# Optimization experiments

Measured on AMD Instinct MI355X. Metric: run time of the kernel, lower is better.

The kernel has to match this reference:

```python
import jax, jax.numpy as jnp
import numpy as np

N_NODES = 100000
N_EDGES = 1600000
IN_FEATS = 128
OUT_FEATS = 64
NEG_SLOPE = 0.2


def setup_inputs() -> dict:
    key = jax.random.key(0)
    k1, k2, k3, k4 = jax.random.split(key, 4)
    feat = jax.random.normal(k1, (N_NODES, IN_FEATS), dtype=jnp.float32)
    # xavier_normal-ish scale for the linear weight (torch Linear stores [out, in])
    W = jax.random.normal(k2, (OUT_FEATS, IN_FEATS), dtype=jnp.float32) * (1.0 / np.sqrt(IN_FEATS))
    src = jax.random.randint(k3, (N_EDGES,), 0, N_NODES, dtype=jnp.int32)
    dst = jax.random.randint(k4, (N_EDGES,), 0, N_NODES, dtype=jnp.int32)
    return {"feat": feat, "W": W, "src": src, "dst": dst}


def reference(feat, W, src, dst):
    n_nodes = feat.shape[0]
    # h = Linear(feat) (no bias)
    h = feat @ W.T                                            # [N, out]
    # update_all(copy_src, sum): h_agg[v] = sum_{(u->v)} h[u]
    h_agg = jax.ops.segment_sum(h[src], dst, num_segments=n_nodes)  # [N, out]
    # NOTE: ndata['h'] was overwritten, so edges see the AGGREGATED features
    e = jnp.sum(h_agg[src] * jnp.tanh(h_agg[dst]), axis=1)   # [E]
    e = jnp.where(e > 0, e, NEG_SLOPE * e)                    # leaky_relu
    # edge_softmax: softmax over incoming edges of each destination node
    m = jax.ops.segment_max(e, dst, num_segments=n_nodes)     # [N]
    ex = jnp.exp(e - m[dst])                                  # [E], stable
    s = jax.ops.segment_sum(ex, dst, num_segments=n_nodes)    # [N]
    e_soft = ex / s[dst]                                      # [E]
    return h_agg, e_soft
```

## Files before the change

### kernel.cpp

```cpp
#include <hip/hip_runtime.h>
#include <math.h>

#define IN_FEATS 128
#define OUT_FEATS 64
#define NEG_SLOPE 0.2f
#define MAXD 256
#define BSH 8
#define BNODES (1 << BSH)
#define CHUNK 8192
#define EID_BITS 21

typedef _Float16 half2_t __attribute__((ext_vector_type(2)));
typedef short bf16x8 __attribute__((ext_vector_type(8)));
typedef float f32x4 __attribute__((ext_vector_type(4)));

__device__ __forceinline__ float bf_lo(unsigned u) { return __uint_as_float(u << 16); }
__device__ __forceinline__ float bf_hi(unsigned u) { return __uint_as_float(u & 0xffff0000u); }
__device__ __forceinline__ unsigned short f2bf(float f) {
  unsigned x = __float_as_uint(f);
  x += 0x7fff + ((x >> 16) & 1);
  return (unsigned short)(x >> 16);
}
template <typename T>
__device__ __forceinline__ unsigned h2u(T h) {
  union { T h; unsigned u; } c; c.h = h; return c.u;
}

__global__ __launch_bounds__(256)
void gemm_h_kernel(const float* __restrict__ feat,
                   const float* __restrict__ W,
                   unsigned short* __restrict__ h16, int n_nodes) {
  const int wid    = (blockIdx.x * blockDim.x + threadIdx.x) >> 6;
  const int lane   = threadIdx.x & 63;
  const int nwaves = (gridDim.x * blockDim.x) >> 6;
  const int r16 = lane & 15;
  const int kb  = lane >> 4;

  bf16x8 wf[4][4];
#pragma unroll
  for (int ot = 0; ot < 4; ++ot) {
#pragma unroll
    for (int kc = 0; kc < 4; ++kc) {
      const float* wp = W + (size_t)(ot * 16 + r16) * IN_FEATS + kc * 32 + kb * 8;
      float4 w0 = *reinterpret_cast<const float4*>(wp);
      float4 w1 = *reinterpret_cast<const float4*>(wp + 4);
      bf16x8 f;
      f[0] = (short)f2bf(w0.x); f[1] = (short)f2bf(w0.y);
      f[2] = (short)f2bf(w0.z); f[3] = (short)f2bf(w0.w);
      f[4] = (short)f2bf(w1.x); f[5] = (short)f2bf(w1.y);
      f[6] = (short)f2bf(w1.z); f[7] = (short)f2bf(w1.w);
      wf[ot][kc] = f;
    }
  }

  const int ntiles = (n_nodes + 15) >> 4;
  for (int t = wid; t < ntiles; t += nwaves) {
    const int n0 = t * 16;
    int row = n0 + r16;
    if (row >= n_nodes) row = n_nodes - 1;
    const float* fp = feat + (size_t)row * IN_FEATS + kb * 8;

    bf16x8 af[4];
#pragma unroll
    for (int kc = 0; kc < 4; ++kc) {
      float4 a0 = *reinterpret_cast<const float4*>(fp + kc * 32);
      float4 a1 = *reinterpret_cast<const float4*>(fp + kc * 32 + 4);
      bf16x8 f;
      f[0] = (short)f2bf(a0.x); f[1] = (short)f2bf(a0.y);
      f[2] = (short)f2bf(a0.z); f[3] = (short)f2bf(a0.w);
      f[4] = (short)f2bf(a1.x); f[5] = (short)f2bf(a1.y);
      f[6] = (short)f2bf(a1.z); f[7] = (short)f2bf(a1.w);
      af[kc] = f;
    }

    f32x4 acc[4];
#pragma unroll
    for (int ot = 0; ot < 4; ++ot) acc[ot] = (f32x4){0.f, 0.f, 0.f, 0.f};
#pragma unroll
    for (int ot = 0; ot < 4; ++ot) {
#pragma unroll
      for (int kc = 0; kc < 4; ++kc) {
        acc[ot] = __builtin_amdgcn_mfma_f32_16x16x32_bf16(af[kc], wf[ot][kc],
                                                          acc[ot], 0, 0, 0);
      }
    }

#pragma unroll
    for (int ot = 0; ot < 4; ++ot) {
#pragma unroll
      for (int reg = 0; reg < 4; ++reg) {
        int node = n0 + (lane >> 4) * 4 + reg;
        if (node < n_nodes)
          h16[(size_t)node * OUT_FEATS + ot * 16 + r16] = f2bf(acc[ot][reg]);
      }
    }
  }
}

__global__ __launch_bounds__(256)
void bhist_kernel(const int* __restrict__ dst, int* __restrict__ bcount,
                  int n_edges, int nbuck) {
  __shared__ int hist[512];
  const int t = threadIdx.x;
  for (int i = t; i < nbuck; i += 256) hist[i] = 0;
  __syncthreads();
  const int n4 = n_edges >> 2;
  const int4* dst4 = reinterpret_cast<const int4*>(dst);
  const int base = blockIdx.x * (CHUNK / 4);
#pragma unroll
  for (int i = 0; i < 8; ++i) {
    int idx = base + t + i * 256;
    if (idx < n4) {
      int4 d = dst4[idx];
      atomicAdd(&hist[d.x >> BSH], 1);
      atomicAdd(&hist[d.y >> BSH], 1);
      atomicAdd(&hist[d.z >> BSH], 1);
      atomicAdd(&hist[d.w >> BSH], 1);
    }
  }
  if (blockIdx.x == 0) {
    for (int e = (n4 << 2) + t; e < n_edges; e += 256)
      atomicAdd(&hist[dst[e] >> BSH], 1);
  }
  __syncthreads();
  for (int i = t; i < nbuck; i += 256)
    if (hist[i]) atomicAdd(&bcount[i], hist[i]);
}

__global__ void bscan_kernel(const int* __restrict__ bcount, int* __restrict__ bbase,
                             int* __restrict__ bcursor, int nbuck, int n_edges) {
  __shared__ int tmp[512];
  const int t = threadIdx.x;
  int v = (t < nbuck) ? bcount[t] : 0;
  tmp[t] = v;
  __syncthreads();
  for (int off = 1; off < 512; off <<= 1) {
    int x = (t >= off) ? tmp[t - off] : 0;
    __syncthreads();
    tmp[t] += x;
    __syncthreads();
  }
  if (t < nbuck) { int excl = tmp[t] - v; bbase[t] = excl; bcursor[t] = excl; }
  if (t == 0) bbase[nbuck] = n_edges;
}

__global__ __launch_bounds__(256)
void bscatter_kernel(const int* __restrict__ src, const int* __restrict__ dst,
                     int* __restrict__ bcursor, int2* __restrict__ tmpe,
                     int n_edges, int nbuck) {
  __shared__ int hist[512];
  __shared__ int basech[512];
  __shared__ int offs[512];
  const int t = threadIdx.x;
  const int n4 = n_edges >> 2;
  const int4* src4 = reinterpret_cast<const int4*>(src);
  const int4* dst4 = reinterpret_cast<const int4*>(dst);
  const int base = blockIdx.x * (CHUNK / 4);
  for (int i = t; i < nbuck; i += 256) { hist[i] = 0; offs[i] = 0; }
  __syncthreads();

  int4 sv[8], dv[8];
#pragma unroll
  for (int i = 0; i < 8; ++i) {
    int idx = base + t + i * 256;
    if (idx < n4) {
      sv[i] = src4[idx];
      dv[i] = dst4[idx];
      atomicAdd(&hist[dv[i].x >> BSH], 1);
      atomicAdd(&hist[dv[i].y >> BSH], 1);
      atomicAdd(&hist[dv[i].z >> BSH], 1);
      atomicAdd(&hist[dv[i].w >> BSH], 1);
    } else {
      dv[i].x = -1;
    }
  }
  if (blockIdx.x == 0) {
    for (int e = (n4 << 2) + t; e < n_edges; e += 256)
      atomicAdd(&hist[dst[e] >> BSH], 1);
  }
  __syncthreads();
  for (int i = t; i < nbuck; i += 256)
    if (hist[i]) basech[i] = atomicAdd(&bcursor[i], hist[i]);
  __syncthreads();

#pragma unroll
  for (int i = 0; i < 8; ++i) {
    if (dv[i].x >= 0) {
      int e0 = (base + t + i * 256) << 2;
      int ss[4] = {sv[i].x, sv[i].y, sv[i].z, sv[i].w};
      int dd[4] = {dv[i].x, dv[i].y, dv[i].z, dv[i].w};
#pragma unroll
      for (int j = 0; j < 4; ++j) {
        int b = dd[j] >> BSH;
        int off = atomicAdd(&offs[b], 1);
        int2 v;
        v.x = ss[j];
        v.y = ((dd[j] & (BNODES - 1)) << EID_BITS) | (e0 + j);
        tmpe[basech[b] + off] = v;
      }
    }
  }
  if (blockIdx.x == 0) {
    for (int e = (n4 << 2) + t; e < n_edges; e += 256) {
      int d = dst[e];
      int b = d >> BSH;
      int off = atomicAdd(&offs[b], 1);
      int2 v;
      v.x = src[e];
      v.y = ((d & (BNODES - 1)) << EID_BITS) | e;
      tmpe[basech[b] + off] = v;
    }
  }
}

__global__ __launch_bounds__(256)
void binB_kernel(const int2* __restrict__ tmpe, const int* __restrict__ bbase,
                 int2* __restrict__ edata, int* __restrict__ row_ptr,
                 int n_nodes, int n_edges) {
  __shared__ int cnt[BNODES];
  __shared__ int cur[BNODES];
  const int b = blockIdx.x;
  const int t = threadIdx.x;
  const int beg = bbase[b], end = bbase[b + 1];

  cnt[t] = 0;
  __syncthreads();
  for (int i = beg + t; i < end; i += 256)
    atomicAdd(&cnt[(tmpe[i].y >> EID_BITS) & (BNODES - 1)], 1);
  __syncthreads();

  int v = cnt[t];
  cur[t] = v;
  __syncthreads();
  for (int off = 1; off < BNODES; off <<= 1) {
    int x = (t >= off) ? cur[t - off] : 0;
    __syncthreads();
    cur[t] += x;
    __syncthreads();
  }
  int excl = cur[t] - v;
  int node = b * BNODES + t;
  if (node < n_nodes) row_ptr[node] = beg + excl;
  if (b == 0 && t == 0) row_ptr[n_nodes] = n_edges;
  __syncthreads();
  cur[t] = beg + excl;
  __syncthreads();

  for (int i = beg + t; i < end; i += 256) {
    int2 p = tmpe[i];
    int l = (p.y >> EID_BITS) & (BNODES - 1);
    int pos = atomicAdd(&cur[l], 1);
    int2 o;
    o.x = p.x;
    o.y = p.y & ((1 << EID_BITS) - 1);
    edata[pos] = o;
  }
}

__global__ void agg_kernel(const unsigned* __restrict__ h16u,
                           const int* __restrict__ row_ptr,
                           const int2* __restrict__ edata, float* __restrict__ h_agg,
                           unsigned* __restrict__ a16u, unsigned* __restrict__ t16u,
                           int n_nodes) {
  int tid  = blockIdx.x * blockDim.x + threadIdx.x;
  int node = tid >> 3;
  int fo   = tid & 7;
  if (node >= n_nodes) return;
  int beg = row_ptr[node], end = row_ptr[node + 1];
  float acc[8] = {0.f, 0.f, 0.f, 0.f, 0.f, 0.f, 0.f, 0.f};
  if (beg < end) {
    uint4 v = *reinterpret_cast<const uint4*>(
        h16u + (unsigned)edata[beg].x * 32u + fo * 4);
    for (int i = beg + 1; i < end; ++i) {
      uint4 vn = *reinterpret_cast<const uint4*>(
          h16u + (unsigned)edata[i].x * 32u + fo * 4);
      acc[0] += bf_lo(v.x); acc[1] += bf_hi(v.x);
      acc[2] += bf_lo(v.y); acc[3] += bf_hi(v.y);
      acc[4] += bf_lo(v.z); acc[5] += bf_hi(v.z);
      acc[6] += bf_lo(v.w); acc[7] += bf_hi(v.w);
      v = vn;
    }
    acc[0] += bf_lo(v.x); acc[1] += bf_hi(v.x);
    acc[2] += bf_lo(v.y); acc[3] += bf_hi(v.y);
    acc[4] += bf_lo(v.z); acc[5] += bf_hi(v.z);
    acc[6] += bf_lo(v.w); acc[7] += bf_hi(v.w);
  }
  float4 a, b;
  a.x = acc[0]; a.y = acc[1]; a.z = acc[2]; a.w = acc[3];
  b.x = acc[4]; b.y = acc[5]; b.z = acc[6]; b.w = acc[7];
  float* out = h_agg + (size_t)node * OUT_FEATS + fo * 8;
  *reinterpret_cast<float4*>(out) = a;
  *reinterpret_cast<float4*>(out + 4) = b;

  uint4 pa;
  pa.x = h2u(__builtin_amdgcn_cvt_pkrtz(acc[0], acc[1]));
  pa.y = h2u(__builtin_amdgcn_cvt_pkrtz(acc[2], acc[3]));
  pa.z = h2u(__builtin_amdgcn_cvt_pkrtz(acc[4], acc[5]));
  pa.w = h2u(__builtin_amdgcn_cvt_pkrtz(acc[6], acc[7]));
  *reinterpret_cast<uint4*>(a16u + (unsigned)node * 32u + fo * 4) = pa;

  uint4 pt;
  pt.x = h2u(__builtin_amdgcn_cvt_pkrtz(tanhf(acc[0]), tanhf(acc[1])));
  pt.y = h2u(__builtin_amdgcn_cvt_pkrtz(tanhf(acc[2]), tanhf(acc[3])));
  pt.z = h2u(__builtin_amdgcn_cvt_pkrtz(tanhf(acc[4]), tanhf(acc[5])));
  pt.w = h2u(__builtin_amdgcn_cvt_pkrtz(tanhf(acc[6]), tanhf(acc[7])));
  *reinterpret_cast<uint4*>(t16u + (unsigned)node * 32u + fo * 4) = pt;
}

__global__ __launch_bounds__(256)
void softmax_kernel(const unsigned* __restrict__ a16u, const unsigned* __restrict__ t16u,
                    const int* __restrict__ row_ptr, const int2* __restrict__ edata,
                    float* __restrict__ e_soft, int n_nodes) {
  __shared__ float ebuf[4][MAXD];
  int wid  = (blockIdx.x * blockDim.x + threadIdx.x) >> 6;
  int lane = threadIdx.x & 63;
  int lw   = threadIdx.x >> 6;
  int eo = lane >> 2;
  int fo = lane & 3;
  if (wid >= n_nodes) return;
  int beg = row_ptr[wid], end = row_ptr[wid + 1];
  int deg = end - beg;
  if (deg == 0) return;

  union U { uint4 u; half2_t h[4]; };
  U tc0, tc1;
  tc0.u = *reinterpret_cast<const uint4*>(t16u + (unsigned)wid * 32u + fo * 8);
  tc1.u = *reinterpret_cast<const uint4*>(t16u + (unsigned)wid * 32u + fo * 8 + 4);

  if (deg <= 32) {
    int eA = eo, eB = 16 + eo;
    int idxA = beg + (eA < deg ? eA : deg - 1);
    int idxB = beg + (eB < deg ? eB : deg - 1);
    int2 edA = edata[idxA];
    int2 edB = edata[idxB];
    U a0A, a1A, a0B, a1B;
    a0A.u = *reinterpret_cast<const uint4*>(a16u + (unsigned)edA.x * 32u + fo * 8);
    a1A.u = *reinterpret_cast<const uint4*>(a16u + (unsigned)edA.x * 32u + fo * 8 + 4);
    a0B.u = *reinterpret_cast<const uint4*>(a16u + (unsigned)edB.x * 32u + fo * 8);
    a1B.u = *reinterpret_cast<const uint4*>(a16u + (unsigned)edB.x * 32u + fo * 8 + 4);

    float dA = 0.f, dB = 0.f;
#pragma unroll
    for (int j = 0; j < 4; ++j) {
      dA = __builtin_amdgcn_fdot2(a0A.h[j], tc0.h[j], dA, false);
      dB = __builtin_amdgcn_fdot2(a0B.h[j], tc0.h[j], dB, false);
    }
#pragma unroll
    for (int j = 0; j < 4; ++j) {
      dA = __builtin_amdgcn_fdot2(a1A.h[j], tc1.h[j], dA, false);
      dB = __builtin_amdgcn_fdot2(a1B.h[j], tc1.h[j], dB, false);
    }
#pragma unroll
    for (int off = 1; off < 4; off <<= 1) {
      dA += __shfl_xor(dA, off, 64);
      dB += __shfl_xor(dB, off, 64);
    }
    dA = dA > 0.f ? dA : NEG_SLOPE * dA;
    dB = dB > 0.f ? dB : NEG_SLOPE * dB;
    float mA = (eA < deg) ? dA : -INFINITY;
    float mB = (eB < deg) ? dB : -INFINITY;
    float mx = fmaxf(mA, mB);
#pragma unroll
    for (int off = 4; off < 64; off <<= 1) mx = fmaxf(mx, __shfl_xor(mx, off, 64));
    float xA = (eA < deg) ? expf(dA - mx) : 0.f;
    float xB = (eB < deg) ? expf(dB - mx) : 0.f;
    float sum = xA + xB;
#pragma unroll
    for (int off = 4; off < 64; off <<= 1) sum += __shfl_xor(sum, off, 64);
    float inv = 1.f / sum;
    if (fo == 0) {
      if (eA < deg) e_soft[edA.y] = xA * inv;
      if (eB < deg) e_soft[edB.y] = xB * inv;
    }
  } else if (deg <= MAXD) {
    for (int i0 = 0; i0 < deg; i0 += 16) {
      int e = i0 + eo;
      int idx = beg + (e < deg ? e : deg - 1);
      int2 ed = edata[idx];
      U a0, a1;
      a0.u = *reinterpret_cast<const uint4*>(a16u + (unsigned)ed.x * 32u + fo * 8);
      a1.u = *reinterpret_cast<const uint4*>(a16u + (unsigned)ed.x * 32u + fo * 8 + 4);
      float d = 0.f;
#pragma unroll
      for (int j = 0; j < 4; ++j) d = __builtin_amdgcn_fdot2(a0.h[j], tc0.h[j], d, false);
#pragma unroll
      for (int j = 0; j < 4; ++j) d = __builtin_amdgcn_fdot2(a1.h[j], tc1.h[j], d, false);
#pragma unroll
      for (int off = 1; off < 4; off <<= 1) d += __shfl_xor(d, off, 64);
      if (fo == 0 && e < deg) {
        d = d > 0.f ? d : NEG_SLOPE * d;
        ebuf[lw][e] = d;
      }
    }
    if (deg <= 64) {
      float sc = (lane < deg) ? ebuf[lw][lane] : -INFINITY;
      float mx = sc;
#pragma unroll
      for (int off = 32; off > 0; off >>= 1) mx = fmaxf(mx, __shfl_xor(mx, off, 64));
      float ex = (lane < deg) ? expf(sc - mx) : 0.f;
      float sum = ex;
#pragma unroll
      for (int off = 32; off > 0; off >>= 1) sum += __shfl_xor(sum, off, 64);
      float inv = 1.f / sum;
      if (lane < deg) e_soft[edata[beg + lane].y] = ex * inv;
    } else {
      float mx = -INFINITY;
      for (int i = lane; i < deg; i += 64) mx = fmaxf(mx, ebuf[lw][i]);
#pragma unroll
      for (int off = 32; off > 0; off >>= 1) mx = fmaxf(mx, __shfl_xor(mx, off, 64));
      float sum = 0.f;
      for (int i = lane; i < deg; i += 64) {
        float ex = expf(ebuf[lw][i] - mx);
        ebuf[lw][i] = ex;
        sum += ex;
      }
#pragma unroll
      for (int off = 32; off > 0; off >>= 1) sum += __shfl_xor(sum, off, 64);
      float inv = 1.f / sum;
      for (int i = lane; i < deg; i += 64) e_soft[edata[beg + i].y] = ebuf[lw][i] * inv;
    }
  } else {
    float mx = -INFINITY;
    for (int i0 = 0; i0 < deg; i0 += 16) {
      int e = i0 + eo;
      int idx = beg + (e < deg ? e : deg - 1);
      int2 ed = edata[idx];
      U a0, a1;
      a0.u = *reinterpret_cast<const uint4*>(a16u + (unsigned)ed.x * 32u + fo * 8);
      a1.u = *reinterpret_cast<const uint4*>(a16u + (unsigned)ed.x * 32u + fo * 8 + 4);
      float d = 0.f;
#pragma unroll
      for (int j = 0; j < 4; ++j) d = __builtin_amdgcn_fdot2(a0.h[j], tc0.h[j], d, false);
#pragma unroll
      for (int j = 0; j < 4; ++j) d = __builtin_amdgcn_fdot2(a1.h[j], tc1.h[j], d, false);
#pragma unroll
      for (int off = 1; off < 4; off <<= 1) d += __shfl_xor(d, off, 64);
      d = d > 0.f ? d : NEG_SLOPE * d;
      if (e >= deg) d = -INFINITY;
#pragma unroll
      for (int off = 4; off < 64; off <<= 1) d = fmaxf(d, __shfl_xor(d, off, 64));
      mx = fmaxf(mx, d);
    }
    float sum = 0.f;
    for (int i0 = 0; i0 < deg; i0 += 16) {
      int e = i0 + eo;
      int idx = beg + (e < deg ? e : deg - 1);
      int2 ed = edata[idx];
      U a0, a1;
      a0.u = *reinterpret_cast<const uint4*>(a16u + (unsigned)ed.x * 32u + fo * 8);
      a1.u = *reinterpret_cast<const uint4*>(a16u + (unsigned)ed.x * 32u + fo * 8 + 4);
      float d = 0.f;
#pragma unroll
      for (int j = 0; j < 4; ++j) d = __builtin_amdgcn_fdot2(a0.h[j], tc0.h[j], d, false);
#pragma unroll
      for (int j = 0; j < 4; ++j) d = __builtin_amdgcn_fdot2(a1.h[j], tc1.h[j], d, false);
#pragma unroll
      for (int off = 1; off < 4; off <<= 1) d += __shfl_xor(d, off, 64);
      d = d > 0.f ? d : NEG_SLOPE * d;
      float ex = (e < deg) ? expf(d - mx) : 0.f;
#pragma unroll
      for (int off = 4; off < 64; off <<= 1) ex += __shfl_xor(ex, off, 64);
      sum += ex;
    }
    float inv = 1.f / sum;
    for (int i0 = 0; i0 < deg; i0 += 16) {
      int e = i0 + eo;
      int idx = beg + (e < deg ? e : deg - 1);
      int2 ed = edata[idx];
      U a0, a1;
      a0.u = *reinterpret_cast<const uint4*>(a16u + (unsigned)ed.x * 32u + fo * 8);
      a1.u = *reinterpret_cast<const uint4*>(a16u + (unsigned)ed.x * 32u + fo * 8 + 4);
      float d = 0.f;
#pragma unroll
      for (int j = 0; j < 4; ++j) d = __builtin_amdgcn_fdot2(a0.h[j], tc0.h[j], d, false);
#pragma unroll
      for (int j = 0; j < 4; ++j) d = __builtin_amdgcn_fdot2(a1.h[j], tc1.h[j], d, false);
#pragma unroll
      for (int off = 1; off < 4; off <<= 1) d += __shfl_xor(d, off, 64);
      d = d > 0.f ? d : NEG_SLOPE * d;
      if (fo == 0 && e < deg) e_soft[ed.y] = expf(d - mx) * inv;
    }
  }
}

extern "C" void kernel_launch(void* const* d_in, const int* in_sizes, int n_in,
                              void* d_out, int out_size, void* d_ws, size_t ws_size,
                              hipStream_t stream) {
  const float* feat = (const float*)d_in[0];
  const float* W    = (const float*)d_in[1];
  const int*   src  = (const int*)d_in[2];
  const int*   dst  = (const int*)d_in[3];
  const int n_nodes = in_sizes[0] / IN_FEATS;
  const int n_edges = in_sizes[2];
  const int nbuck   = (n_nodes + BNODES - 1) >> BSH;

  float* h_agg  = (float*)d_out;
  float* e_soft = (float*)d_out + (size_t)n_nodes * OUT_FEATS;

  unsigned short* h16 = (unsigned short*)d_ws;
  unsigned short* a16 = h16 + (size_t)n_nodes * OUT_FEATS;
  int* bcount   = (int*)(a16 + (size_t)n_nodes * OUT_FEATS);
  int* bbase    = bcount + 513;
  int* bcursor  = bbase + 513;
  int* row_ptr  = bcursor + 512;
  size_t rp_pad = ((size_t)n_nodes + 2) & ~(size_t)1;
  int2* tmpe    = (int2*)(row_ptr + rp_pad);
  int2* edata   = tmpe + n_edges;
  unsigned* t16 = (unsigned*)tmpe;

  const int eb2 = (n_edges + CHUNK - 1) / CHUNK;
  const int wb  = (n_nodes * 64 + 255) / 256;
  const int ab  = (n_nodes * 8 + 255) / 256;

  hipMemsetAsync(bcount, 0, (size_t)nbuck * sizeof(int), stream);

  gemm_h_kernel<<<512, 256, 0, stream>>>(feat, W, h16, n_nodes);

  bhist_kernel<<<eb2, 256, 0, stream>>>(dst, bcount, n_edges, nbuck);
  bscan_kernel<<<1, 512, 0, stream>>>(bcount, bbase, bcursor, nbuck, n_edges);
  bscatter_kernel<<<eb2, 256, 0, stream>>>(src, dst, bcursor, tmpe, n_edges, nbuck);
  binB_kernel<<<nbuck, 256, 0, stream>>>(tmpe, bbase, edata, row_ptr, n_nodes, n_edges);

  agg_kernel<<<ab, 256, 0, stream>>>((const unsigned*)h16, row_ptr, edata,
                                     h_agg, (unsigned*)a16, t16, n_nodes);

  softmax_kernel<<<wb, 256, 0, stream>>>((const unsigned*)a16, (const unsigned*)t16,
                                         row_ptr, edata, e_soft, n_nodes);
}
```

Before: 161.6 us.

## Fuse GEMM with dst histogram launch and process two nodes per softmax wave

Merges the bf16 MFMA linear transform and the destination-bucket histogram into one launch, with extra blocks beyond the GEMM blocks doing the histogram. This removes a launch and lets both independent stages run at the same time. The softmax kernel now gives each wave two consecutive nodes. When both have degree 32 or less, their gathers, dot products and reductions are interleaved for more memory-level parallelism and fewer waves. Other cases fall back to the per-node path. Risks are extra register pressure and divergence between the two nodes.

```diff
diff --git a/kernel.cpp b/kernel.cpp
--- a/kernel.cpp
+++ b/kernel.cpp
@@ -9,6 +9,7 @@
 #define BNODES (1 << BSH)
 #define CHUNK 8192
 #define EID_BITS 21
+#define GEMM_BLOCKS 512
 
 typedef _Float16 half2_t __attribute__((ext_vector_type(2)));
 typedef short bf16x8 __attribute__((ext_vector_type(8)));
@@ -27,12 +28,45 @@
 }
 
 __global__ __launch_bounds__(256)
-void gemm_h_kernel(const float* __restrict__ feat,
-                   const float* __restrict__ W,
-                   unsigned short* __restrict__ h16, int n_nodes) {
-  const int wid    = (blockIdx.x * blockDim.x + threadIdx.x) >> 6;
-  const int lane   = threadIdx.x & 63;
-  const int nwaves = (gridDim.x * blockDim.x) >> 6;
+void gemm_bhist_kernel(const float* __restrict__ feat,
+                       const float* __restrict__ W,
+                       unsigned short* __restrict__ h16, int n_nodes,
+                       const int* __restrict__ dst, int* __restrict__ bcount,
+                       int n_edges, int nbuck) {
+  __shared__ int hist[512];
+  const int t = threadIdx.x;
+
+  if (blockIdx.x >= GEMM_BLOCKS) {
+    for (int i = t; i < nbuck; i += 256) hist[i] = 0;
+    __syncthreads();
+    const int n4 = n_edges >> 2;
+    const int4* dst4 = reinterpret_cast<const int4*>(dst);
+    const int bb = blockIdx.x - GEMM_BLOCKS;
+    const int base = bb * (CHUNK / 4);
+#pragma unroll
+    for (int i = 0; i < 8; ++i) {
+      int idx = base + t + i * 256;
+      if (idx < n4) {
+        int4 d = dst4[idx];
+        atomicAdd(&hist[d.x >> BSH], 1);
+        atomicAdd(&hist[d.y >> BSH], 1);
+        atomicAdd(&hist[d.z >> BSH], 1);
+        atomicAdd(&hist[d.w >> BSH], 1);
+      }
+    }
+    if (bb == 0) {
+      for (int e = (n4 << 2) + t; e < n_edges; e += 256)
+        atomicAdd(&hist[dst[e] >> BSH], 1);
+    }
+    __syncthreads();
+    for (int i = t; i < nbuck; i += 256)
+      if (hist[i]) atomicAdd(&bcount[i], hist[i]);
+    return;
+  }
+
+  const int wid    = (blockIdx.x << 2) + (t >> 6);
+  const int lane   = t & 63;
+  const int nwaves = GEMM_BLOCKS * 4;
   const int r16 = lane & 15;
   const int kb  = lane >> 4;
 
@@ -54,8 +88,8 @@
   }
 
   const int ntiles = (n_nodes + 15) >> 4;
-  for (int t = wid; t < ntiles; t += nwaves) {
-    const int n0 = t * 16;
+  for (int tt = wid; tt < ntiles; tt += nwaves) {
+    const int n0 = tt * 16;
     int row = n0 + r16;
     if (row >= n_nodes) row = n_nodes - 1;
     const float* fp = feat + (size_t)row * IN_FEATS + kb * 8;
@@ -95,36 +129,6 @@
       }
     }
   }
-}
-
-__global__ __launch_bounds__(256)
-void bhist_kernel(const int* __restrict__ dst, int* __restrict__ bcount,
-                  int n_edges, int nbuck) {
-  __shared__ int hist[512];
-  const int t = threadIdx.x;
-  for (int i = t; i < nbuck; i += 256) hist[i] = 0;
-  __syncthreads();
-  const int n4 = n_edges >> 2;
-  const int4* dst4 = reinterpret_cast<const int4*>(dst);
-  const int base = blockIdx.x * (CHUNK / 4);
-#pragma unroll
-  for (int i = 0; i < 8; ++i) {
-    int idx = base + t + i * 256;
-    if (idx < n4) {
-      int4 d = dst4[idx];
-      atomicAdd(&hist[d.x >> BSH], 1);
-      atomicAdd(&hist[d.y >> BSH], 1);
-      atomicAdd(&hist[d.z >> BSH], 1);
-      atomicAdd(&hist[d.w >> BSH], 1);
-    }
-  }
-  if (blockIdx.x == 0) {
-    for (int e = (n4 << 2) + t; e < n_edges; e += 256)
-      atomicAdd(&hist[dst[e] >> BSH], 1);
-  }
-  __syncthreads();
-  for (int i = t; i < nbuck; i += 256)
-    if (hist[i]) atomicAdd(&bcount[i], hist[i]);
 }
 
 __global__ void bscan_kernel(const int* __restrict__ bcount, int* __restrict__ bbase,
@@ -307,21 +311,11 @@
   *reinterpret_cast<uint4*>(t16u + (unsigned)node * 32u + fo * 4) = pt;
 }
 
-__global__ __launch_bounds__(256)
-void softmax_kernel(const unsigned* __restrict__ a16u, const unsigned* __restrict__ t16u,
-                    const int* __restrict__ row_ptr, const int2* __restrict__ edata,
-                    float* __restrict__ e_soft, int n_nodes) {
-  __shared__ float ebuf[4][MAXD];
-  int wid  = (blockIdx.x * blockDim.x + threadIdx.x) >> 6;
-  int lane = threadIdx.x & 63;
-  int lw   = threadIdx.x >> 6;
-  int eo = lane >> 2;
-  int fo = lane & 3;
-  if (wid >= n_nodes) return;
-  int beg = row_ptr[wid], end = row_ptr[wid + 1];
-  int deg = end - beg;
-  if (deg == 0) return;
-
+__device__ __forceinline__
+void softmax_one(const unsigned* __restrict__ a16u, const unsigned* __restrict__ t16u,
+                 const int2* __restrict__ edata, float* __restrict__ e_soft,
+                 float* __restrict__ ebuf_row, int wid, int beg, int deg,
+                 int lane, int eo, int fo) {
   union U { uint4 u; half2_t h[4]; };
   U tc0, tc1;
   tc0.u = *reinterpret_cast<const uint4*>(t16u + (unsigned)wid * 32u + fo * 8);
@@ -373,11 +367,12 @@
       if (eB < deg) e_soft[edB.y] = xB * inv;
     }
   } else if (deg <= MAXD) {
+    union U2 { uint4 u; half2_t h[4]; };
     for (int i0 = 0; i0 < deg; i0 += 16) {
       int e = i0 + eo;
       int idx = beg + (e < deg ? e : deg - 1);
       int2 ed = edata[idx];
-      U a0, a1;
+      U2 a0, a1;
       a0.u = *reinterpret_cast<const uint4*>(a16u + (unsigned)ed.x * 32u + fo * 8);
       a1.u = *reinterpret_cast<const uint4*>(a16u + (unsigned)ed.x * 32u + fo * 8 + 4);
       float d = 0.f;
@@ -389,11 +384,11 @@
       for (int off = 1; off < 4; off <<= 1) d += __shfl_xor(d, off, 64);
       if (fo == 0 && e < deg) {
         d = d > 0.f ? d : NEG_SLOPE * d;
-        ebuf[lw][e] = d;
+        ebuf_row[e] = d;
       }
     }
     if (deg <= 64) {
-      float sc = (lane < deg) ? ebuf[lw][lane] : -INFINITY;
+      float sc = (lane < deg) ? ebuf_row[lane] : -INFINITY;
       float mx = sc;
 #pragma unroll
       for (int off = 32; off > 0; off >>= 1) mx = fmaxf(mx, __shfl_xor(mx, off, 64));
@@ -405,27 +400,28 @@
       if (lane < deg) e_soft[edata[beg + lane].y] = ex * inv;
     } else {
       float mx = -INFINITY;
-      for (int i = lane; i < deg; i += 64) mx = fmaxf(mx, ebuf[lw][i]);
+      for (int i = lane; i < deg; i += 64) mx = fmaxf(mx, ebuf_row[i]);
 #pragma unroll
       for (int off = 32; off > 0; off >>= 1) mx = fmaxf(mx, __shfl_xor(mx, off, 64));
       float sum = 0.f;
       for (int i = lane; i < deg; i += 64) {
-        float ex = expf(ebuf[lw][i] - mx);
-        ebuf[lw][i] = ex;
+        float ex = expf(ebuf_row[i] - mx);
+        ebuf_row[i] = ex;
         sum += ex;
       }
 #pragma unroll
       for (int off = 32; off > 0; off >>= 1) sum += __shfl_xor(sum, off, 64);
       float inv = 1.f / sum;
-      for (int i = lane; i < deg; i += 64) e_soft[edata[beg + i].y] = ebuf[lw][i] * inv;
+      for (int i = lane; i < deg; i += 64) e_soft[edata[beg + i].y] = ebuf_row[i] * inv;
     }
   } else {
+    union U3 { uint4 u; half2_t h[4]; };
     float mx = -INFINITY;
     for (int i0 = 0; i0 < deg; i0 += 16) {
       int e = i0 + eo;
       int idx = beg + (e < deg ? e : deg - 1);
       int2 ed = edata[idx];
-      U a0, a1;
+      U3 a0, a1;
       a0.u = *reinterpret_cast<const uint4*>(a16u + (unsigned)ed.x * 32u + fo * 8);
       a1.u = *reinterpret_cast<const uint4*>(a16u + (unsigned)ed.x * 32u + fo * 8 + 4);
       float d = 0.f;
@@ -446,7 +442,7 @@
       int e = i0 + eo;
       int idx = beg + (e < deg ? e : deg - 1);
       int2 ed = edata[idx];
-      U a0, a1;
+      U3 a0, a1;
       a0.u = *reinterpret_cast<const uint4*>(a16u + (unsigned)ed.x * 32u + fo * 8);
       a1.u = *reinterpret_cast<const uint4*>(a16u + (unsigned)ed.x * 32u + fo * 8 + 4);
       float d = 0.f;
@@ -467,7 +463,7 @@
       int e = i0 + eo;
       int idx = beg + (e < deg ? e : deg - 1);
       int2 ed = edata[idx];
-      U a0, a1;
+      U3 a0, a1;
       a0.u = *reinterpret_cast<const uint4*>(a16u + (unsigned)ed.x * 32u + fo * 8);
       a1.u = *reinterpret_cast<const uint4*>(a16u + (unsigned)ed.x * 32u + fo * 8 + 4);
       float d = 0.f;
@@ -480,6 +476,109 @@
       d = d > 0.f ? d : NEG_SLOPE * d;
       if (fo == 0 && e < deg) e_soft[ed.y] = expf(d - mx) * inv;
     }
+  }
+}
+
+__global__ __launch_bounds__(256)
+void softmax_kernel(const unsigned* __restrict__ a16u, const unsigned* __restrict__ t16u,
+                    const int* __restrict__ row_ptr, const int2* __restrict__ edata,
+                    float* __restrict__ e_soft, int n_nodes) {
+  __shared__ float ebuf[4][MAXD];
+  int wv   = (blockIdx.x * blockDim.x + threadIdx.x) >> 6;
+  int lane = threadIdx.x & 63;
+  int lw   = threadIdx.x >> 6;
+  int eo = lane >> 2;
+  int fo = lane & 3;
+  int n0 = wv * 2;
+  if (n0 >= n_nodes) return;
+  bool has1 = (n0 + 1 < n_nodes);
+
+  int rp0 = row_ptr[n0];
+  int rp1 = row_ptr[n0 + 1];
+  int rp2 = has1 ? row_ptr[n0 + 2] : rp1;
+  int deg0 = rp1 - rp0;
+  int deg1 = rp2 - rp1;
+
+  if (deg0 >= 1 && deg0 <= 32 && has1 && deg1 >= 1 && deg1 <= 32) {
+    union U { uint4 u; half2_t h[4]; };
+    U tc00, tc01, tc10, tc11;
+    tc00.u = *reinterpret_cast<const uint4*>(t16u + (unsigned)n0 * 32u + fo * 8);
+    tc01.u = *reinterpret_cast<const uint4*>(t16u + (unsigned)n0 * 32u + fo * 8 + 4);
+    tc10.u = *reinterpret_cast<const uint4*>(t16u + (unsigned)(n0 + 1) * 32u + fo * 8);
+    tc11.u = *reinterpret_cast<const uint4*>(t16u + (unsigned)(n0 + 1) * 32u + fo * 8 + 4);
+
+    int eA = eo, eB = 16 + eo;
+    int2 ed0A = edata[rp0 + (eA < deg0 ? eA : deg0 - 1)];
+    int2 ed0B = edata[rp0 + (eB < deg0 ? eB : deg0 - 1)];
+    int2 ed1A = edata[rp1 + (eA < deg1 ? eA : deg1 - 1)];
+    int2 ed1B = edata[rp1 + (eB < deg1 ? eB : deg1 - 1)];
+
+    U a00A, a01A, a00B, a01B, a10A, a11A, a10B, a11B;
+    a00A.u = *reinterpret_cast<const uint4*>(a16u + (unsigned)ed0A.x * 32u + fo * 8);
+    a01A.u = *reinterpret_cast<const uint4*>(a16u + (unsigned)ed0A.x * 32u + fo * 8 + 4);
+    a00B.u = *reinterpret_cast<const uint4*>(a16u + (unsigned)ed0B.x * 32u + fo * 8);
+    a01B.u = *reinterpret_cast<const uint4*>(a16u + (unsigned)ed0B.x * 32u + fo * 8 + 4);
+    a10A.u = *reinterpret_cast<const uint4*>(a16u + (unsigned)ed1A.x * 32u + fo * 8);
+    a11A.u = *reinterpret_cast<const uint4*>(a16u + (unsigned)ed1A.x * 32u + fo * 8 + 4);
+    a10B.u = *reinterpret_cast<const uint4*>(a16u + (unsigned)ed1B.x * 32u + fo * 8);
+    a11B.u = *reinterpret_cast<const uint4*>(a16u + (unsigned)ed1B.x * 32u + fo * 8 + 4);
+
+    float d0A = 0.f, d0B = 0.f, d1A = 0.f, d1B = 0.f;
+#pragma unroll
+    for (int j = 0; j < 4; ++j) {
+      d0A = __builtin_amdgcn_fdot2(a00A.h[j], tc00.h[j], d0A, false);
+      d0B = __builtin_amdgcn_fdot2(a00B.h[j], tc00.h[j], d0B, false);
+      d1A = __builtin_amdgcn_fdot2(a10A.h[j], tc10.h[j], d1A, false);
+      d1B = __builtin_amdgcn_fdot2(a10B.h[j], tc10.h[j], d1B, false);
+    }
+#pragma unroll
+    for (int j = 0; j < 4; ++j) {
+      d0A = __builtin_amdgcn_fdot2(a01A.h[j], tc01.h[j], d0A, false);
+      d0B = __builtin_amdgcn_fdot2(a01B.h[j], tc01.h[j], d0B, false);
+      d1A = __builtin_amdgcn_fdot2(a11A.h[j], tc11.h[j], d1A, false);
+      d1B = __builtin_amdgcn_fdot2(a11B.h[j], tc11.h[j], d1B, false);
+    }
+#pragma unroll
+    for (int off = 1; off < 4; off <<= 1) {
+      d0A += __shfl_xor(d0A, off, 64);
+      d0B += __shfl_xor(d0B, off, 64);
+      d1A += __shfl_xor(d1A, off, 64);
+      d1B += __shfl_xor(d1B, off, 64);
+    }
+    d0A = d0A > 0.f ? d0A : NEG_SLOPE * d0A;
+    d0B = d0B > 0.f ? d0B : NEG_SLOPE * d0B;
+    d1A = d1A > 0.f ? d1A : NEG_SLOPE * d1A;
+    d1B = d1B > 0.f ? d1B : NEG_SLOPE * d1B;
+
+    float mx0 = fmaxf((eA < deg0) ? d0A : -INFINITY, (eB < deg0) ? d0B : -INFINITY);
+    float mx1 = fmaxf((eA < deg1) ? d1A : -INFINITY, (eB < deg1) ? d1B : -INFINITY);
+#pragma unroll
+    for (int off = 4; off < 64; off <<= 1) {
+      mx0 = fmaxf(mx0, __shfl_xor(mx0, off, 64));
+      mx1 = fmaxf(mx1, __shfl_xor(mx1, off, 64));
+    }
+    float x0A = (eA < deg0) ? expf(d0A - mx0) : 0.f;
+    float x0B = (eB < deg0) ? expf(d0B - mx0) : 0.f;
+    float x1A = (eA < deg1) ? expf(d1A - mx1) : 0.f;
+    float x1B = (eB < deg1) ? expf(d1B - mx1) : 0.f;
+    float s0 = x0A + x0B, s1 = x1A + x1B;
+#pragma unroll
+    for (int off = 4; off < 64; off <<= 1) {
+      s0 += __shfl_xor(s0, off, 64);
+      s1 += __shfl_xor(s1, off, 64);
+    }
+    float inv0 = 1.f / s0, inv1 = 1.f / s1;
+    if (fo == 0) {
+      if (eA < deg0) e_soft[ed0A.y] = x0A * inv0;
+      if (eB < deg0) e_soft[ed0B.y] = x0B * inv0;
+      if (eA < deg1) e_soft[ed1A.y] = x1A * inv1;
+      if (eB < deg1) e_soft[ed1B.y] = x1B * inv1;
+    }
+  } else {
+    if (deg0 > 0)
+      softmax_one(a16u, t16u, edata, e_soft, ebuf[lw], n0, rp0, deg0, lane, eo, fo);
+    if (has1 && deg1 > 0)
+      softmax_one(a16u, t16u, edata, e_soft, ebuf[lw], n0 + 1, rp1, deg1, lane, eo, fo);
   }
 }
 
@@ -509,14 +608,15 @@
   unsigned* t16 = (unsigned*)tmpe;
 
   const int eb2 = (n_edges + CHUNK - 1) / CHUNK;
-  const int wb  = (n_nodes * 64 + 255) / 256;
   const int ab  = (n_nodes * 8 + 255) / 256;
+  const int nwave2 = (n_nodes + 1) / 2;
+  const int sb  = (nwave2 * 64 + 255) / 256;
 
   hipMemsetAsync(bcount, 0, (size_t)nbuck * sizeof(int), stream);
 
-  gemm_h_kernel<<<512, 256, 0, stream>>>(feat, W, h16, n_nodes);
-
-  bhist_kernel<<<eb2, 256, 0, stream>>>(dst, bcount, n_edges, nbuck);
+  gemm_bhist_kernel<<<GEMM_BLOCKS + eb2, 256, 0, stream>>>(
+      feat, W, h16, n_nodes, dst, bcount, n_edges, nbuck);
+
   bscan_kernel<<<1, 512, 0, stream>>>(bcount, bbase, bcursor, nbuck, n_edges);
   bscatter_kernel<<<eb2, 256, 0, stream>>>(src, dst, bcursor, tmpe, n_edges, nbuck);
   binB_kernel<<<nbuck, 256, 0, stream>>>(tmpe, bbase, edata, row_ptr, n_nodes, n_edges);
@@ -524,6 +624,6 @@
   agg_kernel<<<ab, 256, 0, stream>>>((const unsigned*)h16, row_ptr, edata,
                                      h_agg, (unsigned*)a16, t16, n_nodes);
 
-  softmax_kernel<<<wb, 256, 0, stream>>>((const unsigned*)a16, (const unsigned*)t16,
+  softmax_kernel<<<sb, 256, 0, stream>>>((const unsigned*)a16, (const unsigned*)t16,
                                          row_ptr, edata, e_soft, n_nodes);
 }
```

Result: faster. 157.0 us (-2.8%).
